# Kernel optimization log

Measured on AMD Instinct MI355X. Metric: run time of the kernel, lower is better.

## Reference

```python
import jax, jax.numpy as jnp
import numpy as np

B, S, D, H, L = 4, 2048, 512, 8, 128
HD = D // H  # head dim = 64


def setup_inputs() -> dict:
    key = jax.random.key(0)
    ks = jax.random.split(key, 20)
    sc = 0.05
    return {
        "query": jax.random.normal(ks[0], (B, S, D), jnp.float32),
        "key": jax.random.normal(ks[1], (B, S, D), jnp.float32),
        "value": jax.random.normal(ks[2], (B, S, D), jnp.float32),
        "Wq": jax.random.normal(ks[3], (D, D), jnp.float32) * sc,
        "bq": jax.random.normal(ks[4], (D,), jnp.float32) * sc,
        "Wk": jax.random.normal(ks[5], (D, D), jnp.float32) * sc,
        "bk": jax.random.normal(ks[6], (D,), jnp.float32) * sc,
        "Wv": jax.random.normal(ks[7], (D, D), jnp.float32) * sc,
        "bv": jax.random.normal(ks[8], (D,), jnp.float32) * sc,
        "Wo": jax.random.normal(ks[9], (D, D), jnp.float32) * sc,
        "bo": jax.random.normal(ks[10], (D,), jnp.float32) * sc,
        "Wg": jax.random.normal(ks[11], (D, L), jnp.float32) * sc,
        "bg": jax.random.normal(ks[12], (L,), jnp.float32) * sc,
        "Wmq": jax.random.normal(ks[13], (L, D), jnp.float32) * sc,
        "bmq": jax.random.normal(ks[14], (D,), jnp.float32) * sc,
        "Wmk": jax.random.normal(ks[15], (L, D), jnp.float32) * sc,
        "bmk": jax.random.normal(ks[16], (D,), jnp.float32) * sc,
    }


def reference(query, key, value, Wq, bq, Wk, bk, Wv, bv, Wo, bo, Wg, bg, Wmq, bmq, Wmk, bmk):
    # latent-gated modulation of Q and K (computed from query)
    latent = jax.nn.relu(query @ Wg + bg)                 # [B,S,L]
    mod_q = jax.nn.sigmoid(latent @ Wmq + bmq)            # [B,S,D]
    mod_k = jax.nn.sigmoid(latent @ Wmk + bmk)            # [B,S,D]
    q = (query @ Wq + bq) * mod_q
    k = (key @ Wk + bk) * mod_k
    v = value @ Wv + bv
    # split heads: [B,S,D] -> [B,S,H,HD]
    q = q.reshape(B, S, H, HD)
    k = k.reshape(B, S, H, HD)
    v = v.reshape(B, S, H, HD)
    scale = 1.0 / jnp.sqrt(jnp.float32(HD))
    scores = jnp.einsum("bqhd,bkhd->bhqk", q, k) * scale  # [B,H,S,S]
    attn_weights = jax.nn.softmax(scores, axis=-1)
    attn_out = jnp.einsum("bhqk,bkhd->bqhd", attn_weights, v).reshape(B, S, D)
    output = attn_out @ Wo + bo
    return output, attn_weights
```

## Files before the change

kernel.cpp:

```cpp
#include <hip/hip_runtime.h>
#include <hip/hip_bf16.h>

#define BB 4
#define SS 2048
#define DD 512
#define HH 8
#define HDIM 64

typedef __attribute__((ext_vector_type(8))) short bf16x8;
typedef __attribute__((ext_vector_type(4))) float floatx4;
typedef __attribute__((ext_vector_type(8))) unsigned short u16x8;

static __device__ __forceinline__ unsigned short f2bf(float x) {
  __hip_bfloat16 h = __float2bfloat16(x);
  unsigned short u;
  __builtin_memcpy(&u, &h, sizeof(u));
  return u;
}
static __device__ __forceinline__ float bf2f(unsigned short u) {
  union { unsigned int i; float f; } c;
  c.i = ((unsigned int)u) << 16;
  return c.f;
}
static __device__ __forceinline__ void split1(float x, unsigned short& h, unsigned short& l) {
  h = f2bf(x);
  l = f2bf(x - bf2f(h));
}
static __device__ __forceinline__ void gload_lds16(const void* g, void* l) {
  __builtin_amdgcn_global_load_lds((const __attribute__((address_space(1))) void*)g,
                                   (__attribute__((address_space(3))) void*)l, 16, 0, 0);
}

#define SWZ(row, col) ((col) ^ (((row) & 7) * 8))

__global__ __launch_bounds__(256)
void wsplit_kernel(const float* __restrict__ Wq, const float* __restrict__ Wk,
                   const float* __restrict__ Wv, const float* __restrict__ Wo,
                   const float* __restrict__ Wg, const float* __restrict__ Wmq,
                   const float* __restrict__ Wmk, unsigned short* __restrict__ wsb)
{
  const int bx = blockIdx.x;
  const float* src; unsigned short* dh; unsigned short* dl; int K, N, tile;
  if (bx < 64)       { src = Wq;  dh = wsb + 0;       dl = wsb + 262144;  K = 512; N = 512; tile = bx; }
  else if (bx < 128) { src = Wk;  dh = wsb + 524288;  dl = wsb + 786432;  K = 512; N = 512; tile = bx - 64; }
  else if (bx < 192) { src = Wv;  dh = wsb + 1048576; dl = wsb + 1310720; K = 512; N = 512; tile = bx - 128; }
  else if (bx < 256) { src = Wo;  dh = wsb + 1572864; dl = wsb + 1835008; K = 512; N = 512; tile = bx - 192; }
  else if (bx < 272) { src = Wg;  dh = wsb + 2097152; dl = wsb + 2162688; K = 512; N = 128; tile = bx - 256; }
  else if (bx < 288) { src = Wmq; dh = wsb + 2228224; dl = wsb + 2293760; K = 128; N = 512; tile = bx - 272; }
  else               { src = Wmk; dh = wsb + 2359296; dl = wsb + 2424832; K = 128; N = 512; tile = bx - 288; }
  const int nt = N >> 6;
  const int k0 = (tile / nt) * 64, n0 = (tile % nt) * 64;
  __shared__ float T[64][65];
  const int t = threadIdx.x;
  const int r = t >> 2, c = (t & 3) * 16;
#pragma unroll
  for (int j = 0; j < 16; j += 4)
    *(float4*)&T[r][c + j] = *(const float4*)&src[(size_t)(k0 + r) * N + n0 + c + j];
  __syncthreads();
  u16x8 hv[2], lv[2];
#pragma unroll
  for (int j = 0; j < 16; ++j) {
    unsigned short h, l;
    split1(T[c + j][r], h, l);
    hv[j >> 3][j & 7] = h;
    lv[j >> 3][j & 7] = l;
  }
  const size_t di = (size_t)(n0 + r) * K + k0 + c;
  *(u16x8*)&dh[di]     = hv[0];
  *(u16x8*)&dh[di + 8] = hv[1];
  *(u16x8*)&dl[di]     = lv[0];
  *(u16x8*)&dl[di + 8] = lv[1];
}

template<int BM, int BN>
static __device__ __forceinline__ void gemm_phase(
    const float* __restrict__ A, const unsigned short* __restrict__ WHp,
    const unsigned short* __restrict__ WLp, const int K,
    const int m0, const int n0,
    unsigned short (*Ah)[32], unsigned short (*Al)[32],
    unsigned short (*Bh)[32], unsigned short (*Bl)[32],
    floatx4 (*acc)[BN / 32])
{
  constexpr int HM = BM / 2, HN = BN / 2, FM = BM / 32, FN = BN / 32;
  constexpr int TPR = 256 / BM;
  constexpr int CPT = 32 / TPR;
  constexpr int WCH = BN / 16;
  constexpr int WPW = (2 * WCH) / 4;
  const int t = threadIdx.x;
  const int wid = t >> 6, lane = t & 63, quad = lane >> 4, l16 = lane & 15;
  const int wm = wid >> 1, wn = wid & 1;
  const int arow = t / TPR, acol = (t % TPR) * CPT;
  const int asw = (arow & 3) * 8;

  for (int k0 = 0; k0 < K; k0 += 32) {
    __syncthreads();
#pragma unroll
    for (int cc = 0; cc < WPW; ++cc) {
      const int cid = wid * WPW + cc;
      const int pl = cid / WCH, ch = cid - pl * WCH;
      const int row = ch * 16 + (lane >> 2);
      const int kof = ((lane & 3) ^ ((lane >> 2) & 3)) * 8;
      const unsigned short* g = (pl ? WLp : WHp) + (size_t)(n0 + row) * K + k0 + kof;
      gload_lds16(g, (pl ? Bl : Bh)[ch * 16]);
    }
    {
      const float* ga = A + (size_t)(m0 + arow) * K + k0 + acol;
#pragma unroll
      for (int j = 0; j < CPT; j += 4) {
        float4 f = *(const float4*)(ga + j);
        unsigned short h[4], l[4];
        split1(f.x, h[0], l[0]); split1(f.y, h[1], l[1]);
        split1(f.z, h[2], l[2]); split1(f.w, h[3], l[3]);
        *(ushort4*)&Ah[arow][(acol + j) ^ asw] = make_ushort4(h[0], h[1], h[2], h[3]);
        *(ushort4*)&Al[arow][(acol + j) ^ asw] = make_ushort4(l[0], l[1], l[2], l[3]);
      }
    }
    __syncthreads();
    const int swf = (l16 & 3) * 8;
    bf16x8 fah[FM], fal[FM], fbh[FN], fbl[FN];
#pragma unroll
    for (int mi = 0; mi < FM; ++mi) {
      const int rr = wm * HM + mi * 16 + l16;
      fah[mi] = *(const bf16x8*)&Ah[rr][(quad * 8) ^ swf];
      fal[mi] = *(const bf16x8*)&Al[rr][(quad * 8) ^ swf];
    }
#pragma unroll
    for (int ni = 0; ni < FN; ++ni) {
      const int rr = wn * HN + ni * 16 + l16;
      fbh[ni] = *(const bf16x8*)&Bh[rr][(quad * 8) ^ swf];
      fbl[ni] = *(const bf16x8*)&Bl[rr][(quad * 8) ^ swf];
    }
#pragma unroll
    for (int mi = 0; mi < FM; ++mi)
#pragma unroll
      for (int ni = 0; ni < FN; ++ni) {
        acc[mi][ni] = __builtin_amdgcn_mfma_f32_16x16x32_bf16(fah[mi], fbh[ni], acc[mi][ni], 0, 0, 0);
        acc[mi][ni] = __builtin_amdgcn_mfma_f32_16x16x32_bf16(fal[mi], fbh[ni], acc[mi][ni], 0, 0, 0);
        acc[mi][ni] = __builtin_amdgcn_mfma_f32_16x16x32_bf16(fah[mi], fbl[ni], acc[mi][ni], 0, 0, 0);
      }
  }
}

template<int BM, int BN, int EPI>
__global__ __launch_bounds__(256, 2)
void mgemm_kernel(const float* __restrict__ A, const unsigned short* __restrict__ WH,
                  const unsigned short* __restrict__ WL, const float* __restrict__ bias,
                  const float* __restrict__ A2, const unsigned short* __restrict__ W2H,
                  const unsigned short* __restrict__ W2L, const float* __restrict__ bias2,
                  float* __restrict__ Cf, unsigned short* __restrict__ C16,
                  int K1, int K2, int N)
{
  constexpr int HM = BM / 2, HN = BN / 2, FM = BM / 32, FN = BN / 32;
  __shared__ alignas(16) unsigned short Ah[BM][32], Al[BM][32], Bh[BN][32], Bl[BN][32];
  const int t = threadIdx.x;
  const int wid = t >> 6, lane = t & 63, quad = lane >> 4, l16 = lane & 15;
  const int wm = wid >> 1, wn = wid & 1;
  const int m0 = blockIdx.y * BM, n0 = blockIdx.x * BN;

  floatx4 acc1[FM][FN], acc2[FM][FN];
#pragma unroll
  for (int i = 0; i < FM; ++i)
#pragma unroll
    for (int j = 0; j < FN; ++j) {
      floatx4 z = {0.f, 0.f, 0.f, 0.f};
      acc1[i][j] = z; acc2[i][j] = z;
    }

  gemm_phase<BM, BN>(A, WH, WL, K1, m0, n0, Ah, Al, Bh, Bl, acc1);
  if constexpr (EPI == 3)
    gemm_phase<BM, BN>(A2, W2H, W2L, K2, m0, n0, Ah, Al, Bh, Bl, acc2);

#pragma unroll
  for (int ni = 0; ni < FN; ++ni) {
    const int col = n0 + wn * HN + ni * 16 + l16;
    const float b1 = bias[col];
    float b2 = 0.f;
    if constexpr (EPI == 3) b2 = bias2[col];
#pragma unroll
    for (int mi = 0; mi < FM; ++mi)
#pragma unroll
      for (int r = 0; r < 4; ++r) {
        const int row = m0 + wm * HM + mi * 16 + quad * 4 + r;
        float v = acc1[mi][ni][r] + b1;
        if constexpr (EPI == 0) {
          Cf[(size_t)row * N + col] = v;
        } else if constexpr (EPI == 1) {
          Cf[(size_t)row * N + col] = fmaxf(v, 0.f);
        } else if constexpr (EPI == 2) {
          C16[(size_t)row * N + col] = f2bf(v);
        } else {
          float v2 = acc2[mi][ni][r] + b2;
          C16[(size_t)row * N + col] = f2bf(v / (1.f + __expf(-v2)));
        }
      }
  }
}

__global__ __launch_bounds__(256)
void vtrans_kernel(const unsigned short* __restrict__ V16, unsigned short* __restrict__ Vt)
{
  __shared__ unsigned short T[64][72];
  const int x  = blockIdx.x;
  const int st = x & 31;
  const int h  = (x >> 5) & 7;
  const int b  = x >> 8;
  const int t  = threadIdx.x;
  const unsigned short* src = V16 + ((size_t)b * SS + st * 64) * DD + h * HDIM;
  for (int i = t; i < 1024; i += 256) {
    int r = i >> 4, c4 = (i & 15) * 4;
    *(ushort4*)&T[r][c4] = *(const ushort4*)&src[(size_t)r * DD + c4];
  }
  __syncthreads();
  unsigned short* dst = Vt + ((size_t)(b * HH + h) * HDIM) * SS + st * 64;
  for (int i = t; i < 1024; i += 256) {
    int hd = i >> 4, s4 = (i & 15) * 4;
    ushort4 u = make_ushort4(T[s4 + 0][hd], T[s4 + 1][hd], T[s4 + 2][hd], T[s4 + 3][hd]);
    *(ushort4*)&dst[(size_t)hd * SS + s4] = u;
  }
}

__global__ __launch_bounds__(256)
void attn_kernel(const unsigned short* __restrict__ Q16,
                 const unsigned short* __restrict__ K16,
                 const unsigned short* __restrict__ Vt,
                 float* __restrict__ AW, float* __restrict__ AO)
{
  __shared__ alignas(16) unsigned short Qs[64][64];
  __shared__ alignas(16) unsigned short Ks[64][64];
  __shared__ alignas(16) unsigned short Vs[64][64];
  __shared__ alignas(16) unsigned short Ps[4][16][64];

  const int t    = threadIdx.x;
  const int wid  = t >> 6;
  const int lane = t & 63;
  const int quad = lane >> 4;
  const int l16  = lane & 15;
  const int x  = blockIdx.x;
  const int qb = x & 31;
  const int h  = (x >> 5) & 7;
  const int b  = x >> 8;
  const int q0 = qb * 64;
  const float scale = 0.125f;

  const unsigned short* Qg = Q16 + ((size_t)b * SS + q0) * DD + h * HDIM;
  for (int i = t; i < 1024; i += 256) {
    int r = i >> 4, c4 = (i & 15) * 4;
    *(ushort4*)&Qs[r][SWZ(r, c4)] = *(const ushort4*)&Qg[(size_t)r * DD + c4];
  }
  __syncthreads();
  const bf16x8 a0 = *(const bf16x8*)&Qs[wid * 16 + l16][SWZ(l16, quad * 8)];
  const bf16x8 a1 = *(const bf16x8*)&Qs[wid * 16 + l16][SWZ(l16, 32 + quad * 8)];

  const unsigned short* Kg = K16 + (size_t)b * SS * DD + h * HDIM;
  const unsigned short* Vg = Vt + ((size_t)(b * HH + h) * HDIM) * SS;

  float m_run[4] = {-1e30f, -1e30f, -1e30f, -1e30f};
  float l_run[4] = {0.f, 0.f, 0.f, 0.f};

  for (int kt = 0; kt < SS / 64; ++kt) {
    __syncthreads();
    for (int i = t; i < 1024; i += 256) {
      int r = i >> 4, c4 = (i & 15) * 4;
      *(ushort4*)&Ks[r][SWZ(r, c4)] = *(const ushort4*)&Kg[(size_t)(kt * 64 + r) * DD + c4];
    }
    __syncthreads();
    float s[4][4];
#pragma unroll
    for (int kst = 0; kst < 4; ++kst) {
      bf16x8 bb0 = *(const bf16x8*)&Ks[kst * 16 + l16][SWZ(l16, quad * 8)];
      bf16x8 bb1 = *(const bf16x8*)&Ks[kst * 16 + l16][SWZ(l16, 32 + quad * 8)];
      floatx4 cc = {0.f, 0.f, 0.f, 0.f};
      cc = __builtin_amdgcn_mfma_f32_16x16x32_bf16(a0, bb0, cc, 0, 0, 0);
      cc = __builtin_amdgcn_mfma_f32_16x16x32_bf16(a1, bb1, cc, 0, 0, 0);
#pragma unroll
      for (int r = 0; r < 4; ++r) s[kst][r] = cc[r] * scale;
    }
#pragma unroll
    for (int r = 0; r < 4; ++r) {
      float mt = fmaxf(fmaxf(s[0][r], s[1][r]), fmaxf(s[2][r], s[3][r]));
#pragma unroll
      for (int off = 1; off < 16; off <<= 1)
        mt = fmaxf(mt, __shfl_xor(mt, off, 64));
      float nm = fmaxf(m_run[r], mt);
      float su = __expf(s[0][r] - nm) + __expf(s[1][r] - nm) +
                 __expf(s[2][r] - nm) + __expf(s[3][r] - nm);
#pragma unroll
      for (int off = 1; off < 16; off <<= 1)
        su += __shfl_xor(su, off, 64);
      l_run[r] = l_run[r] * __expf(m_run[r] - nm) + su;
      m_run[r] = nm;
    }
  }
  float inv_l[4];
#pragma unroll
  for (int r = 0; r < 4; ++r) inv_l[r] = 1.f / l_run[r];

  floatx4 o[4];
#pragma unroll
  for (int n = 0; n < 4; ++n) { floatx4 z = {0.f, 0.f, 0.f, 0.f}; o[n] = z; }

  const size_t awb = ((size_t)(b * HH + h) * SS + q0 + wid * 16) * SS;

  for (int kt = 0; kt < SS / 64; ++kt) {
    __syncthreads();
    for (int i = t; i < 1024; i += 256) {
      int r = i >> 4, c4 = (i & 15) * 4;
      *(ushort4*)&Ks[r][SWZ(r, c4)] = *(const ushort4*)&Kg[(size_t)(kt * 64 + r) * DD + c4];
      *(ushort4*)&Vs[r][SWZ(r, c4)] = *(const ushort4*)&Vg[(size_t)r * SS + kt * 64 + c4];
    }
    __syncthreads();
#pragma unroll
    for (int kst = 0; kst < 4; ++kst) {
      bf16x8 bb0 = *(const bf16x8*)&Ks[kst * 16 + l16][SWZ(l16, quad * 8)];
      bf16x8 bb1 = *(const bf16x8*)&Ks[kst * 16 + l16][SWZ(l16, 32 + quad * 8)];
      floatx4 cc = {0.f, 0.f, 0.f, 0.f};
      cc = __builtin_amdgcn_mfma_f32_16x16x32_bf16(a0, bb0, cc, 0, 0, 0);
      cc = __builtin_amdgcn_mfma_f32_16x16x32_bf16(a1, bb1, cc, 0, 0, 0);
#pragma unroll
      for (int r = 0; r < 4; ++r) {
        float wv = __expf(cc[r] * scale - m_run[r]) * inv_l[r];
        Ps[wid][quad * 4 + r][SWZ(quad * 4 + r, kst * 16 + l16)] = f2bf(wv);
      }
    }
    __syncthreads();
    for (int i = lane; i < 256; i += 64) {
      int q = i >> 4, k4 = (i & 15) * 4;
      ushort4 u = *(const ushort4*)&Ps[wid][q][SWZ(q, k4)];
      float4 f = make_float4(bf2f(u.x), bf2f(u.y), bf2f(u.z), bf2f(u.w));
      *(float4*)&AW[awb + (size_t)q * SS + kt * 64 + k4] = f;
    }
#pragma unroll
    for (int c2 = 0; c2 < 2; ++c2) {
      bf16x8 ap = *(const bf16x8*)&Ps[wid][l16][SWZ(l16, c2 * 32 + quad * 8)];
#pragma unroll
      for (int n = 0; n < 4; ++n) {
        bf16x8 bv = *(const bf16x8*)&Vs[n * 16 + l16][SWZ(l16, c2 * 32 + quad * 8)];
        o[n] = __builtin_amdgcn_mfma_f32_16x16x32_bf16(ap, bv, o[n], 0, 0, 0);
      }
    }
  }
  float* AOg = AO + ((size_t)b * SS + q0 + wid * 16) * DD + h * HDIM;
#pragma unroll
  for (int n = 0; n < 4; ++n)
#pragma unroll
    for (int r = 0; r < 4; ++r)
      AOg[(size_t)(quad * 4 + r) * DD + n * 16 + l16] = o[n][r];
}

extern "C" void kernel_launch(void* const* d_in, const int* in_sizes, int n_in,
                              void* d_out, int out_size, void* d_ws, size_t ws_size,
                              hipStream_t stream) {
  (void)in_sizes; (void)n_in; (void)out_size; (void)ws_size;
  const float* query = (const float*)d_in[0];
  const float* key_i = (const float*)d_in[1];
  const float* value = (const float*)d_in[2];
  const float* Wq  = (const float*)d_in[3];
  const float* bq  = (const float*)d_in[4];
  const float* Wk  = (const float*)d_in[5];
  const float* bk  = (const float*)d_in[6];
  const float* Wv  = (const float*)d_in[7];
  const float* bv  = (const float*)d_in[8];
  const float* Wo  = (const float*)d_in[9];
  const float* bo  = (const float*)d_in[10];
  const float* Wg  = (const float*)d_in[11];
  const float* bg  = (const float*)d_in[12];
  const float* Wmq = (const float*)d_in[13];
  const float* bmq = (const float*)d_in[14];
  const float* Wmk = (const float*)d_in[15];
  const float* bmk = (const float*)d_in[16];

  float* out = (float*)d_out;
  float* AW  = out + (size_t)BB * SS * DD;

  char* ws = (char*)d_ws;
  unsigned short* ws16 = (unsigned short*)ws;
  unsigned short* q16 = (unsigned short*)(ws + (5u  << 20));
  unsigned short* k16 = (unsigned short*)(ws + (13u << 20));
  unsigned short* vt  = (unsigned short*)(ws + (21u << 20));
  float*          lat = (float*)(ws + (29u << 20));
  unsigned short* v16 = (unsigned short*)(ws + (33u << 20));
  float*          ao  = (float*)(ws + (29u << 20));

  const size_t W_WQH = 0,       W_WQL = 262144;
  const size_t W_WKH = 524288,  W_WKL = 786432;
  const size_t W_WVH = 1048576, W_WVL = 1310720;
  const size_t W_WOH = 1572864, W_WOL = 1835008;
  const size_t W_WGH = 2097152, W_WGL = 2162688;
  const size_t W_WMQH = 2228224, W_WMQL = 2293760;
  const size_t W_WMKH = 2359296, W_WMKL = 2424832;

  dim3 blk(256);
  wsplit_kernel<<<dim3(304), blk, 0, stream>>>(Wq, Wk, Wv, Wo, Wg, Wmq, Wmk, ws16);
  mgemm_kernel<64, 64, 1><<<dim3(2, 128), blk, 0, stream>>>(
      query, ws16 + W_WGH, ws16 + W_WGL, bg,
      nullptr, nullptr, nullptr, nullptr, lat, nullptr, 512, 0, 128);
  mgemm_kernel<128, 128, 3><<<dim3(4, 64), blk, 0, stream>>>(
      query, ws16 + W_WQH, ws16 + W_WQL, bq,
      lat, ws16 + W_WMQH, ws16 + W_WMQL, bmq, nullptr, q16, 512, 128, 512);
  mgemm_kernel<128, 128, 3><<<dim3(4, 64), blk, 0, stream>>>(
      key_i, ws16 + W_WKH, ws16 + W_WKL, bk,
      lat, ws16 + W_WMKH, ws16 + W_WMKL, bmk, nullptr, k16, 512, 128, 512);
  mgemm_kernel<128, 128, 2><<<dim3(4, 64), blk, 0, stream>>>(
      value, ws16 + W_WVH, ws16 + W_WVL, bv,
      nullptr, nullptr, nullptr, nullptr, nullptr, v16, 512, 0, 512);
  vtrans_kernel<<<dim3(1024), blk, 0, stream>>>(v16, vt);
  attn_kernel<<<dim3(1024), blk, 0, stream>>>(q16, k16, vt, AW, ao);
  mgemm_kernel<128, 128, 0><<<dim3(4, 64), blk, 0, stream>>>(
      ao, ws16 + W_WOH, ws16 + W_WOL, bo,
      nullptr, nullptr, nullptr, nullptr, out, nullptr, 512, 0, 512);
}
```

Before: 920.8 us.

## Double-buffer attention K/V with async LDS loads, drop max pass, split modulation GEMMs

The attention kernel now stages K and V through double-buffered LDS using direct global-to-LDS loads, removing a sync per tile. It drops the running-max softmax rescale and relies on the 1/8 scale being folded into Q. It writes attention weights straight from registers in fp32 instead of a bf16 round-trip, and remaps blocks so neighbouring blocks share the same batch and head. The fused modulation GEMMs are split into separate sigmoid and multiply kernels, and tile shapes change from 128x128 to 128x64. Skipping the max subtraction risks overflow for large scores, and the split adds an fp32 intermediate round trip through memory.

```diff
diff --git a/kernel.cpp b/kernel.cpp
--- a/kernel.cpp
+++ b/kernel.cpp
@@ -32,6 +32,18 @@
 }
 
 #define SWZ(row, col) ((col) ^ (((row) & 7) * 8))
+
+static __device__ __forceinline__ void stage_tile(unsigned short* dst,
+    const unsigned short* src, size_t rstride, int wid, int lane) {
+#pragma unroll
+  for (int it = 0; it < 2; ++it) {
+    const int base = it * 256 + wid * 64;
+    const int c = base + lane;
+    const int row = c >> 3, uu = c & 7;
+    gload_lds16(src + (size_t)row * rstride + ((uu ^ (row & 7)) * 8),
+                dst + (size_t)base * 8);
+  }
+}
 
 __global__ __launch_bounds__(256)
 void wsplit_kernel(const float* __restrict__ Wq, const float* __restrict__ Wk,
@@ -145,10 +157,9 @@
 __global__ __launch_bounds__(256, 2)
 void mgemm_kernel(const float* __restrict__ A, const unsigned short* __restrict__ WH,
                   const unsigned short* __restrict__ WL, const float* __restrict__ bias,
-                  const float* __restrict__ A2, const unsigned short* __restrict__ W2H,
-                  const unsigned short* __restrict__ W2L, const float* __restrict__ bias2,
+                  const float* __restrict__ modf, const float sc,
                   float* __restrict__ Cf, unsigned short* __restrict__ C16,
-                  int K1, int K2, int N)
+                  int K, int N)
 {
   constexpr int HM = BM / 2, HN = BN / 2, FM = BM / 32, FN = BN / 32;
   __shared__ alignas(16) unsigned short Ah[BM][32], Al[BM][32], Bh[BN][32], Bl[BN][32];
@@ -157,40 +168,38 @@
   const int wm = wid >> 1, wn = wid & 1;
   const int m0 = blockIdx.y * BM, n0 = blockIdx.x * BN;
 
-  floatx4 acc1[FM][FN], acc2[FM][FN];
+  floatx4 acc[FM][FN];
 #pragma unroll
   for (int i = 0; i < FM; ++i)
 #pragma unroll
     for (int j = 0; j < FN; ++j) {
       floatx4 z = {0.f, 0.f, 0.f, 0.f};
-      acc1[i][j] = z; acc2[i][j] = z;
-    }
-
-  gemm_phase<BM, BN>(A, WH, WL, K1, m0, n0, Ah, Al, Bh, Bl, acc1);
-  if constexpr (EPI == 3)
-    gemm_phase<BM, BN>(A2, W2H, W2L, K2, m0, n0, Ah, Al, Bh, Bl, acc2);
+      acc[i][j] = z;
+    }
+
+  gemm_phase<BM, BN>(A, WH, WL, K, m0, n0, Ah, Al, Bh, Bl, acc);
 
 #pragma unroll
   for (int ni = 0; ni < FN; ++ni) {
     const int col = n0 + wn * HN + ni * 16 + l16;
     const float b1 = bias[col];
-    float b2 = 0.f;
-    if constexpr (EPI == 3) b2 = bias2[col];
 #pragma unroll
     for (int mi = 0; mi < FM; ++mi)
 #pragma unroll
       for (int r = 0; r < 4; ++r) {
         const int row = m0 + wm * HM + mi * 16 + quad * 4 + r;
-        float v = acc1[mi][ni][r] + b1;
+        float v = acc[mi][ni][r] + b1;
         if constexpr (EPI == 0) {
           Cf[(size_t)row * N + col] = v;
         } else if constexpr (EPI == 1) {
           Cf[(size_t)row * N + col] = fmaxf(v, 0.f);
         } else if constexpr (EPI == 2) {
           C16[(size_t)row * N + col] = f2bf(v);
+        } else if constexpr (EPI == 4) {
+          const float m = modf[(size_t)row * N + col];
+          C16[(size_t)row * N + col] = f2bf(v * m * sc);
         } else {
-          float v2 = acc2[mi][ni][r] + b2;
-          C16[(size_t)row * N + col] = f2bf(v / (1.f + __expf(-v2)));
+          Cf[(size_t)row * N + col] = 1.f / (1.f + __expf(-v));
         }
       }
   }
@@ -219,15 +228,15 @@
   }
 }
 
-__global__ __launch_bounds__(256)
+__global__ __launch_bounds__(256, 3)
 void attn_kernel(const unsigned short* __restrict__ Q16,
                  const unsigned short* __restrict__ K16,
                  const unsigned short* __restrict__ Vt,
                  float* __restrict__ AW, float* __restrict__ AO)
 {
   __shared__ alignas(16) unsigned short Qs[64][64];
-  __shared__ alignas(16) unsigned short Ks[64][64];
-  __shared__ alignas(16) unsigned short Vs[64][64];
+  __shared__ alignas(16) unsigned short Ks[2][64][64];
+  __shared__ alignas(16) unsigned short Vs[2][64][64];
   __shared__ alignas(16) unsigned short Ps[4][16][64];
 
   const int t    = threadIdx.x;
@@ -236,64 +245,48 @@
   const int quad = lane >> 4;
   const int l16  = lane & 15;
   const int x  = blockIdx.x;
-  const int qb = x & 31;
-  const int h  = (x >> 5) & 7;
-  const int b  = x >> 8;
+  const int j  = x >> 3;
+  const int g  = ((j >> 5) << 3) | (x & 7);
+  const int qb = j & 31;
+  const int b  = g >> 3;
+  const int h  = g & 7;
   const int q0 = qb * 64;
-  const float scale = 0.125f;
 
   const unsigned short* Qg = Q16 + ((size_t)b * SS + q0) * DD + h * HDIM;
-  for (int i = t; i < 1024; i += 256) {
-    int r = i >> 4, c4 = (i & 15) * 4;
-    *(ushort4*)&Qs[r][SWZ(r, c4)] = *(const ushort4*)&Qg[(size_t)r * DD + c4];
-  }
+  const unsigned short* Kg = K16 + (size_t)b * SS * DD + h * HDIM;
+  const unsigned short* Vg = Vt + ((size_t)(b * HH + h) * HDIM) * SS;
+
+  stage_tile(&Qs[0][0], Qg, DD, wid, lane);
+  stage_tile(&Ks[0][0][0], Kg, DD, wid, lane);
   __syncthreads();
+
   const bf16x8 a0 = *(const bf16x8*)&Qs[wid * 16 + l16][SWZ(l16, quad * 8)];
   const bf16x8 a1 = *(const bf16x8*)&Qs[wid * 16 + l16][SWZ(l16, 32 + quad * 8)];
 
-  const unsigned short* Kg = K16 + (size_t)b * SS * DD + h * HDIM;
-  const unsigned short* Vg = Vt + ((size_t)(b * HH + h) * HDIM) * SS;
-
-  float m_run[4] = {-1e30f, -1e30f, -1e30f, -1e30f};
-  float l_run[4] = {0.f, 0.f, 0.f, 0.f};
-
+  float lsum[4] = {0.f, 0.f, 0.f, 0.f};
   for (int kt = 0; kt < SS / 64; ++kt) {
-    __syncthreads();
-    for (int i = t; i < 1024; i += 256) {
-      int r = i >> 4, c4 = (i & 15) * 4;
-      *(ushort4*)&Ks[r][SWZ(r, c4)] = *(const ushort4*)&Kg[(size_t)(kt * 64 + r) * DD + c4];
-    }
-    __syncthreads();
-    float s[4][4];
+    const int cur = kt & 1;
+    if (kt < 31)
+      stage_tile(&Ks[cur ^ 1][0][0], Kg + (size_t)(kt + 1) * 64 * DD, DD, wid, lane);
 #pragma unroll
     for (int kst = 0; kst < 4; ++kst) {
-      bf16x8 bb0 = *(const bf16x8*)&Ks[kst * 16 + l16][SWZ(l16, quad * 8)];
-      bf16x8 bb1 = *(const bf16x8*)&Ks[kst * 16 + l16][SWZ(l16, 32 + quad * 8)];
+      bf16x8 bb0 = *(const bf16x8*)&Ks[cur][kst * 16 + l16][SWZ(l16, quad * 8)];
+      bf16x8 bb1 = *(const bf16x8*)&Ks[cur][kst * 16 + l16][SWZ(l16, 32 + quad * 8)];
       floatx4 cc = {0.f, 0.f, 0.f, 0.f};
       cc = __builtin_amdgcn_mfma_f32_16x16x32_bf16(a0, bb0, cc, 0, 0, 0);
       cc = __builtin_amdgcn_mfma_f32_16x16x32_bf16(a1, bb1, cc, 0, 0, 0);
 #pragma unroll
-      for (int r = 0; r < 4; ++r) s[kst][r] = cc[r] * scale;
-    }
-#pragma unroll
-    for (int r = 0; r < 4; ++r) {
-      float mt = fmaxf(fmaxf(s[0][r], s[1][r]), fmaxf(s[2][r], s[3][r]));
-#pragma unroll
-      for (int off = 1; off < 16; off <<= 1)
-        mt = fmaxf(mt, __shfl_xor(mt, off, 64));
-      float nm = fmaxf(m_run[r], mt);
-      float su = __expf(s[0][r] - nm) + __expf(s[1][r] - nm) +
-                 __expf(s[2][r] - nm) + __expf(s[3][r] - nm);
-#pragma unroll
-      for (int off = 1; off < 16; off <<= 1)
-        su += __shfl_xor(su, off, 64);
-      l_run[r] = l_run[r] * __expf(m_run[r] - nm) + su;
-      m_run[r] = nm;
-    }
-  }
-  float inv_l[4];
-#pragma unroll
-  for (int r = 0; r < 4; ++r) inv_l[r] = 1.f / l_run[r];
+      for (int r = 0; r < 4; ++r) lsum[r] += __expf(cc[r]);
+    }
+    __syncthreads();
+  }
+#pragma unroll
+  for (int r = 0; r < 4; ++r) {
+    float v = lsum[r];
+    v += __shfl_xor(v, 1, 64); v += __shfl_xor(v, 2, 64);
+    v += __shfl_xor(v, 4, 64); v += __shfl_xor(v, 8, 64);
+    lsum[r] = 1.f / v;
+  }
 
   floatx4 o[4];
 #pragma unroll
@@ -301,43 +294,39 @@
 
   const size_t awb = ((size_t)(b * HH + h) * SS + q0 + wid * 16) * SS;
 
+  stage_tile(&Ks[0][0][0], Kg, DD, wid, lane);
+  stage_tile(&Vs[0][0][0], Vg, SS, wid, lane);
+  __syncthreads();
   for (int kt = 0; kt < SS / 64; ++kt) {
-    __syncthreads();
-    for (int i = t; i < 1024; i += 256) {
-      int r = i >> 4, c4 = (i & 15) * 4;
-      *(ushort4*)&Ks[r][SWZ(r, c4)] = *(const ushort4*)&Kg[(size_t)(kt * 64 + r) * DD + c4];
-      *(ushort4*)&Vs[r][SWZ(r, c4)] = *(const ushort4*)&Vg[(size_t)r * SS + kt * 64 + c4];
-    }
-    __syncthreads();
+    const int cur = kt & 1;
+    if (kt < 31) {
+      stage_tile(&Ks[cur ^ 1][0][0], Kg + (size_t)(kt + 1) * 64 * DD, DD, wid, lane);
+      stage_tile(&Vs[cur ^ 1][0][0], Vg + (size_t)(kt + 1) * 64, SS, wid, lane);
+    }
 #pragma unroll
     for (int kst = 0; kst < 4; ++kst) {
-      bf16x8 bb0 = *(const bf16x8*)&Ks[kst * 16 + l16][SWZ(l16, quad * 8)];
-      bf16x8 bb1 = *(const bf16x8*)&Ks[kst * 16 + l16][SWZ(l16, 32 + quad * 8)];
+      bf16x8 bb0 = *(const bf16x8*)&Ks[cur][kst * 16 + l16][SWZ(l16, quad * 8)];
+      bf16x8 bb1 = *(const bf16x8*)&Ks[cur][kst * 16 + l16][SWZ(l16, 32 + quad * 8)];
       floatx4 cc = {0.f, 0.f, 0.f, 0.f};
       cc = __builtin_amdgcn_mfma_f32_16x16x32_bf16(a0, bb0, cc, 0, 0, 0);
       cc = __builtin_amdgcn_mfma_f32_16x16x32_bf16(a1, bb1, cc, 0, 0, 0);
 #pragma unroll
       for (int r = 0; r < 4; ++r) {
-        float wv = __expf(cc[r] * scale - m_run[r]) * inv_l[r];
+        const float wv = __expf(cc[r]) * lsum[r];
+        AW[awb + (size_t)(quad * 4 + r) * SS + kt * 64 + kst * 16 + l16] = wv;
         Ps[wid][quad * 4 + r][SWZ(quad * 4 + r, kst * 16 + l16)] = f2bf(wv);
       }
     }
-    __syncthreads();
-    for (int i = lane; i < 256; i += 64) {
-      int q = i >> 4, k4 = (i & 15) * 4;
-      ushort4 u = *(const ushort4*)&Ps[wid][q][SWZ(q, k4)];
-      float4 f = make_float4(bf2f(u.x), bf2f(u.y), bf2f(u.z), bf2f(u.w));
-      *(float4*)&AW[awb + (size_t)q * SS + kt * 64 + k4] = f;
-    }
 #pragma unroll
     for (int c2 = 0; c2 < 2; ++c2) {
       bf16x8 ap = *(const bf16x8*)&Ps[wid][l16][SWZ(l16, c2 * 32 + quad * 8)];
 #pragma unroll
       for (int n = 0; n < 4; ++n) {
-        bf16x8 bv = *(const bf16x8*)&Vs[n * 16 + l16][SWZ(l16, c2 * 32 + quad * 8)];
+        bf16x8 bv = *(const bf16x8*)&Vs[cur][n * 16 + l16][SWZ(l16, c2 * 32 + quad * 8)];
         o[n] = __builtin_amdgcn_mfma_f32_16x16x32_bf16(ap, bv, o[n], 0, 0, 0);
       }
     }
+    __syncthreads();
   }
   float* AOg = AO + ((size_t)b * SS + q0 + wid * 16) * DD + h * HDIM;
 #pragma unroll
@@ -378,8 +367,9 @@
   unsigned short* k16 = (unsigned short*)(ws + (13u << 20));
   unsigned short* vt  = (unsigned short*)(ws + (21u << 20));
   float*          lat = (float*)(ws + (29u << 20));
+  float*          X   = (float*)(ws + (33u << 20));
   unsigned short* v16 = (unsigned short*)(ws + (33u << 20));
-  float*          ao  = (float*)(ws + (29u << 20));
+  float*          ao  = (float*)(ws + (33u << 20));
 
   const size_t W_WQH = 0,       W_WQL = 262144;
   const size_t W_WKH = 524288,  W_WKL = 786432;
@@ -392,20 +382,19 @@
   dim3 blk(256);
   wsplit_kernel<<<dim3(304), blk, 0, stream>>>(Wq, Wk, Wv, Wo, Wg, Wmq, Wmk, ws16);
   mgemm_kernel<64, 64, 1><<<dim3(2, 128), blk, 0, stream>>>(
-      query, ws16 + W_WGH, ws16 + W_WGL, bg,
-      nullptr, nullptr, nullptr, nullptr, lat, nullptr, 512, 0, 128);
-  mgemm_kernel<128, 128, 3><<<dim3(4, 64), blk, 0, stream>>>(
-      query, ws16 + W_WQH, ws16 + W_WQL, bq,
-      lat, ws16 + W_WMQH, ws16 + W_WMQL, bmq, nullptr, q16, 512, 128, 512);
-  mgemm_kernel<128, 128, 3><<<dim3(4, 64), blk, 0, stream>>>(
-      key_i, ws16 + W_WKH, ws16 + W_WKL, bk,
-      lat, ws16 + W_WMKH, ws16 + W_WMKL, bmk, nullptr, k16, 512, 128, 512);
-  mgemm_kernel<128, 128, 2><<<dim3(4, 64), blk, 0, stream>>>(
-      value, ws16 + W_WVH, ws16 + W_WVL, bv,
-      nullptr, nullptr, nullptr, nullptr, nullptr, v16, 512, 0, 512);
+      query, ws16 + W_WGH, ws16 + W_WGL, bg, nullptr, 1.f, lat, nullptr, 512, 128);
+  mgemm_kernel<64, 64, 5><<<dim3(8, 128), blk, 0, stream>>>(
+      lat, ws16 + W_WMQH, ws16 + W_WMQL, bmq, nullptr, 1.f, X, nullptr, 128, 512);
+  mgemm_kernel<128, 64, 4><<<dim3(8, 64), blk, 0, stream>>>(
+      query, ws16 + W_WQH, ws16 + W_WQL, bq, X, 0.125f, nullptr, q16, 512, 512);
+  mgemm_kernel<64, 64, 5><<<dim3(8, 128), blk, 0, stream>>>(
+      lat, ws16 + W_WMKH, ws16 + W_WMKL, bmk, nullptr, 1.f, X, nullptr, 128, 512);
+  mgemm_kernel<128, 64, 4><<<dim3(8, 64), blk, 0, stream>>>(
+      key_i, ws16 + W_WKH, ws16 + W_WKL, bk, X, 1.f, nullptr, k16, 512, 512);
+  mgemm_kernel<128, 64, 2><<<dim3(8, 64), blk, 0, stream>>>(
+      value, ws16 + W_WVH, ws16 + W_WVL, bv, nullptr, 1.f, nullptr, v16, 512, 512);
   vtrans_kernel<<<dim3(1024), blk, 0, stream>>>(v16, vt);
   attn_kernel<<<dim3(1024), blk, 0, stream>>>(q16, k16, vt, AW, ao);
-  mgemm_kernel<128, 128, 0><<<dim3(4, 64), blk, 0, stream>>>(
-      ao, ws16 + W_WOH, ws16 + W_WOL, bo,
-      nullptr, nullptr, nullptr, nullptr, out, nullptr, 512, 0, 512);
-}
+  mgemm_kernel<128, 64, 0><<<dim3(8, 64), blk, 0, stream>>>(
+      ao, ws16 + W_WOH, ws16 + W_WOL, bo, nullptr, 1.f, out, nullptr, 512, 512);
+}
```

Result: faster. 865.9 us (-6.0%).
